# Kernel tuning notes

Hardware: AMD Instinct MI355X
Metric: run time of the kernel (lower is better)

## Reference

```python
import jax, jax.numpy as jnp
import numpy as np

D = 196  # input_size
B = 262144

def _lrelu(x):
    return jax.nn.leaky_relu(x, 0.1)

def setup_inputs() -> dict:
    key = jax.random.key(0)
    ks = jax.random.split(key, 24)
    def w(k, shape):
        fan_in = shape[0]
        return jax.random.uniform(k, shape, jnp.float32, -1.0, 1.0) / np.sqrt(fan_in)
    inp = {}
    inp['x'] = jax.random.normal(ks[0], (B, D), jnp.float32)
    # feature attention: D -> D//2 -> D
    inp['fa_w1'] = w(ks[1], (D, D // 2)); inp['fa_b1'] = jnp.zeros((D // 2,), jnp.float32)
    inp['fa_w2'] = w(ks[2], (D // 2, D)); inp['fa_b2'] = jnp.zeros((D,), jnp.float32)
    # encoder: D -> 96 -> 64 -> 32 -> (8 mean, 8 logvar)
    inp['e_w1'] = w(ks[3], (D, 96)); inp['e_b1'] = jnp.zeros((96,), jnp.float32)
    inp['e_w2'] = w(ks[4], (96, 64)); inp['e_b2'] = jnp.zeros((64,), jnp.float32)
    inp['e_w3'] = w(ks[5], (64, 32)); inp['e_b3'] = jnp.zeros((32,), jnp.float32)
    inp['e_wm'] = w(ks[6], (32, 8)); inp['e_bm'] = jnp.zeros((8,), jnp.float32)
    inp['e_wv'] = w(ks[7], (32, 8)); inp['e_bv'] = jnp.zeros((8,), jnp.float32)
    # decoder: 8 -> 32 -> 64 -> 96 -> D
    inp['d_w1'] = w(ks[8], (8, 32)); inp['d_b1'] = jnp.zeros((32,), jnp.float32)
    inp['d_w2'] = w(ks[9], (32, 64)); inp['d_b2'] = jnp.zeros((64,), jnp.float32)
    inp['d_w3'] = w(ks[10], (64, 96)); inp['d_b3'] = jnp.zeros((96,), jnp.float32)
    inp['d_w4'] = w(ks[11], (96, D)); inp['d_b4'] = jnp.zeros((D,), jnp.float32)
    # layer attention: 3 -> 3 + softmax
    inp['la_w'] = w(ks[12], (3, 3)); inp['la_b'] = jnp.zeros((3,), jnp.float32)
    return inp

def _decoder(z, d_w1, d_b1, d_w2, d_b2, d_w3, d_b3, d_w4, d_b4):
    z = _lrelu(z @ d_w1 + d_b1)
    z = _lrelu(z @ d_w2 + d_b2)
    z = _lrelu(z @ d_w3 + d_b3)
    return jax.nn.sigmoid(z @ d_w4 + d_b4)

def reference(x, fa_w1, fa_b1, fa_w2, fa_b2,
              e_w1, e_b1, e_w2, e_b2, e_w3, e_b3, e_wm, e_bm, e_wv, e_bv,
              d_w1, d_b1, d_w2, d_b2, d_w3, d_b3, d_w4, d_b4,
              la_w, la_b):
    # feature attention
    a = jax.nn.sigmoid(jnp.tanh(x @ fa_w1 + fa_b1) @ fa_w2 + fa_b2)
    attn_weights = a / (jnp.mean(a, axis=1, keepdims=True) + 1e-8)
    x_attn = x * attn_weights
    # encoder
    h1 = _lrelu(x_attn @ e_w1 + e_b1)   # [B,96]
    h2 = _lrelu(h1 @ e_w2 + e_b2)       # [B,64]
    h3 = _lrelu(h2 @ e_w3 + e_b3)       # [B,32]
    mean = h3 @ e_wm + e_bm             # [B,8]
    log_var = h3 @ e_wv + e_bv          # [B,8]
    std = jnp.exp(0.5 * log_var)
    # reparameterize (fresh eps per call, matching torch.randn_like per call)
    ek = jax.random.split(jax.random.key(42), 4)
    z = mean + jax.random.normal(ek[0], mean.shape, mean.dtype) * std
    recon = _decoder(z, d_w1, d_b1, d_w2, d_b2, d_w3, d_b3, d_w4, d_b4)
    # per-layer losses: decoder re-invoked with fresh reparam each time
    layer_losses = []
    for i, h in enumerate((h1, h2, h3)):
        zi = mean + jax.random.normal(ek[i + 1], mean.shape, mean.dtype) * std
        lr = _decoder(zi, d_w1, d_b1, d_w2, d_b2, d_w3, d_b3, d_w4, d_b4)
        layer_losses.append(jnp.mean((h - lr[:, :h.shape[1]]) ** 2, axis=1))
    layer_losses = jnp.stack(layer_losses, axis=1)  # [B,3]
    layer_attn = jax.nn.softmax(layer_losses @ la_w + la_b, axis=-1)
    weighted_layer_loss = jnp.mean(jnp.sum(layer_losses * layer_attn, axis=1))
    return (recon, mean, log_var, attn_weights, weighted_layer_loss)
```

## Files before the change

### kernel.cpp

```cpp
#include <hip/hip_runtime.h>
#include <cstdint>
#include <cstddef>


typedef short short8 __attribute__((ext_vector_type(8)));
typedef float f32x4  __attribute__((ext_vector_type(4)));
typedef float f32x16 __attribute__((ext_vector_type(16)));
typedef unsigned short u16x4 __attribute__((ext_vector_type(4)));
typedef uint32_t u32x2 __attribute__((ext_vector_type(2)));

static constexpr size_t OFF_RECON = 0;
static constexpr size_t OFF_MEAN  = (size_t)262144 * 196;
static constexpr size_t OFF_LOGV  = OFF_MEAN + (size_t)262144 * 8;
static constexpr size_t OFF_ATTN  = OFF_LOGV + (size_t)262144 * 8;
static constexpr size_t OFF_LOSS  = OFF_ATTN + (size_t)262144 * 196;

static constexpr int WS_FA1 = 0;
static constexpr int WS_FA2 = 26624;
static constexpr int WS_E1  = 51712;
static constexpr int WS_E2  = 71680;
static constexpr int WS_E3  = 78848;
static constexpr int WS_EMV = 81408;
static constexpr int WS_D1  = 82944;
static constexpr int WS_D2  = 83456;
static constexpr int WS_D3  = 86528;
static constexpr int WS_D4  = 94208;
static constexpr int WS_TOT = 119296;

static constexpr int XA0 = 0;
static constexpr int T0  = 6912;
static constexpr int TA0 = 10752;
static constexpr int H1o = 6912;
static constexpr int H2o = 10752;
static constexpr int H3o = 13568;
static constexpr int D1o = 15360;
static constexpr int D2o = 3840;
static constexpr int D3o = 0;
static constexpr int Zo  = 17152;
static constexpr int SU_TOT = 19200;
static constexpr int SF_MEAN = 0, SF_STD = 256, SF_ATT = 512, SF_LL = 544;
static constexpr int SF_TOT = 640;

static constexpr unsigned short BF_ONE = 0x3F80;

struct Params {
  const float* x;
  const float* fa_w1; const float* fa_b1; const float* fa_w2; const float* fa_b2;
  const float* e_w1;  const float* e_b1;  const float* e_w2;  const float* e_b2;
  const float* e_w3;  const float* e_b3;  const float* e_wm;  const float* e_bm;
  const float* e_wv;  const float* e_bv;
  const float* d_w1;  const float* d_b1;  const float* d_w2;  const float* d_b2;
  const float* d_w3;  const float* d_b3;  const float* d_w4;  const float* d_b4;
  const float* la_w;  const float* la_b;
  float* out;
  uint32_t key[8];
};

__host__ __device__ inline void tf2x32(uint32_t k0, uint32_t k1, uint32_t x0, uint32_t x1,
                                       uint32_t& o0, uint32_t& o1)
{
  uint32_t kx = k0 ^ k1 ^ 0x1BD11BDAu;
  uint32_t a = x0 + k0, b = x1 + k1;
#define TF_R(r) { a += b; b = (b << (r)) | (b >> (32 - (r))); b ^= a; }
  TF_R(13) TF_R(15) TF_R(26) TF_R(6)
  a += k1; b += kx + 1u;
  TF_R(17) TF_R(29) TF_R(16) TF_R(24)
  a += kx; b += k0 + 2u;
  TF_R(13) TF_R(15) TF_R(26) TF_R(6)
  a += k0; b += k1 + 3u;
  TF_R(17) TF_R(29) TF_R(16) TF_R(24)
  a += k1; b += kx + 4u;
  TF_R(13) TF_R(15) TF_R(26) TF_R(6)
  a += kx; b += k0 + 5u;
#undef TF_R
  o0 = a; o1 = b;
}

__device__ __forceinline__ float jax_normal(uint32_t k0, uint32_t k1, uint32_t idx)
{
  uint32_t o0, o1;
  tf2x32(k0, k1, 0u, idx, o0, o1);
  uint32_t bits = o0 ^ o1;
  float f = __uint_as_float((bits >> 9) | 0x3f800000u) - 1.0f;
  const float lo = -0.99999994f;
  float u = fmaf(f, 2.0f, lo);
  u = fmaxf(u, lo);
  float w = -log1pf(-u * u);
  float p;
  if (w < 5.0f) {
    w -= 2.5f;
    p = 2.81022636e-08f;
    p = fmaf(p, w, 3.43273939e-07f);
    p = fmaf(p, w, -3.5233877e-06f);
    p = fmaf(p, w, -4.39150654e-06f);
    p = fmaf(p, w, 0.00021858087f);
    p = fmaf(p, w, -0.00125372503f);
    p = fmaf(p, w, -0.00417768164f);
    p = fmaf(p, w, 0.246640727f);
    p = fmaf(p, w, 1.50140941f);
  } else {
    w = sqrtf(w) - 3.0f;
    p = -0.000200214257f;
    p = fmaf(p, w, 0.000100950558f);
    p = fmaf(p, w, 0.00134934322f);
    p = fmaf(p, w, -0.00367342844f);
    p = fmaf(p, w, 0.00573950773f);
    p = fmaf(p, w, -0.0076224613f);
    p = fmaf(p, w, 0.00943887047f);
    p = fmaf(p, w, 1.00167406f);
    p = fmaf(p, w, 2.83297682f);
  }
  return 1.41421356237f * (p * u);
}

__host__ __device__ __forceinline__ unsigned short f2b(float f) {
  uint32_t u = __float_as_uint(f);
  uint32_t r = u + 0x7fffu + ((u >> 16) & 1u);
  return (unsigned short)(r >> 16);
}
__device__ __forceinline__ float b2f(unsigned short hh) {
  return __uint_as_float(((uint32_t)hh) << 16);
}
__device__ __forceinline__ uint32_t cvt_pk(float lo, float hi) {
  uint32_t r;
  asm("v_cvt_pk_bf16_f32 %0, %1, %2" : "=v"(r) : "v"(lo), "v"(hi));
  return r;
}
__device__ __forceinline__ float rcpf(float x) { return __builtin_amdgcn_rcpf(x); }
__device__ __forceinline__ float sigm(float x) { return rcpf(1.0f + __expf(-x)); }
__device__ __forceinline__ float tanh_fast(float x) {
  float xc = fminf(fmaxf(x, -8.0f), 8.0f);
  float t = __expf(2.0f * xc);
  return (t - 1.0f) * rcpf(t + 1.0f);
}

__global__ void pack_w(Params p, unsigned short* ws)
{
  int e = blockIdx.x * 256 + threadIdx.x;
  if (e >= WS_TOT) return;
  int base, KS, K, N, special = 0;
  const float* src = nullptr; const float* bias = nullptr;
  if (e < WS_FA2)      { base = WS_FA1; KS = 13; K = 196; N = 98;  src = p.fa_w1; bias = p.fa_b1; }
  else if (e < WS_E1)  { base = WS_FA2; KS = 7;  K = 98;  N = 196; src = p.fa_w2; bias = p.fa_b2; }
  else if (e < WS_E2)  { base = WS_E1;  KS = 13; K = 196; N = 96;  src = p.e_w1;  bias = p.e_b1; }
  else if (e < WS_E3)  { base = WS_E2;  KS = 7;  K = 96;  N = 64;  src = p.e_w2;  bias = p.e_b2; }
  else if (e < WS_EMV) { base = WS_E3;  KS = 5;  K = 64;  N = 32;  src = p.e_w3;  bias = p.e_b3; }
  else if (e < WS_D1)  { base = WS_EMV; KS = 3;  K = 32;  N = 16;  special = 1; }
  else if (e < WS_D2)  { base = WS_D1;  KS = 1;  K = 8;   N = 32;  src = p.d_w1;  bias = p.d_b1; }
  else if (e < WS_D3)  { base = WS_D2;  KS = 3;  K = 32;  N = 64;  src = p.d_w2;  bias = p.d_b2; }
  else if (e < WS_D4)  { base = WS_D3;  KS = 5;  K = 64;  N = 96;  src = p.d_w3;  bias = p.d_b3; }
  else                 { base = WS_D4;  KS = 7;  K = 96;  N = 196; src = p.d_w4;  bias = p.d_b4; }
  int local = e - base;
  int j = local & 7, lane = (local >> 3) & 63, t = local >> 9;
  int ksi = t % KS, ft = t / KS;
  int k = ksi * 16 + ((lane >> 5) << 3) + j;
  int n = ft * 32 + (lane & 31);
  float v = 0.f;
  if (n < N) {
    if (k < K)       v = special ? ((n < 8) ? p.e_wm[k * 8 + n] : p.e_wv[k * 8 + (n - 8)])
                                 : src[k * N + n];
    else if (k == K) v = special ? ((n < 8) ? p.e_bm[n] : p.e_bv[n - 8]) : bias[n];
  }
  ws[e] = f2b(v);
}

template<int KS>
__device__ __forceinline__ f32x16 tile32(const unsigned short* A, int sA,
                                         const unsigned short* W, int ft, int lane)
{
  f32x16 a0 = {}, a1 = {};
  const unsigned short* ar = A + (lane & 31) * sA + ((lane >> 5) << 3);
  const unsigned short* wp = W + (size_t)(ft * KS * 64 + lane) * 8;
  constexpr int CH = (KS > 8) ? ((KS + 1) / 2) : KS;
#pragma unroll
  for (int c = 0; c < KS; c += CH) {
    short8 w8[CH], a8[CH];
#pragma unroll
    for (int i = 0; i < CH; ++i) {
      if (c + i < KS) {
        w8[i] = *(const short8*)(wp + (c + i) * 512);
        a8[i] = *(const short8*)(ar + (c + i) * 16);
      }
    }
#pragma unroll
    for (int i = 0; i < CH; ++i) {
      if (c + i < KS) {
        if (i & 1) a1 = __builtin_amdgcn_mfma_f32_32x32x16_bf16(w8[i], a8[i], a1, 0, 0, 0);
        else       a0 = __builtin_amdgcn_mfma_f32_32x32x16_bf16(w8[i], a8[i], a0, 0, 0, 0);
      }
    }
  }
  if (KS > 1) a0 += a1;
  return a0;
}

template<int KS, int NFT, int SA, int SD>
__device__ __forceinline__ void layer_lrelu(unsigned short* sU, int aOff, int dOff,
                                            const unsigned short* W, int lane, int wv)
{
  const int m = lane & 31, h = lane >> 5;
  for (int t = wv; t < NFT; t += 4) {
    f32x16 acc = tile32<KS>(sU + aOff, SA, W, t, lane);
#pragma unroll
    for (int g = 0; g < 4; ++g) {
      int fb = t * 32 + 8 * g + 4 * h;
      float v0 = fmaxf(acc[4*g+0], 0.1f*acc[4*g+0]);
      float v1 = fmaxf(acc[4*g+1], 0.1f*acc[4*g+1]);
      float v2 = fmaxf(acc[4*g+2], 0.1f*acc[4*g+2]);
      float v3 = fmaxf(acc[4*g+3], 0.1f*acc[4*g+3]);
      u32x2 pk = { cvt_pk(v0, v1), cvt_pk(v2, v3) };
      *(u32x2*)&sU[dOff + m * SD + fb] = pk;
    }
  }
}

__launch_bounds__(256, 4)
__global__ void vae_fused(Params p, const unsigned short* ws)
{
  __shared__ unsigned short sU[SU_TOT];
  __shared__ float sF[SF_TOT];

  const int tid = threadIdx.x;
  const int lane = tid & 63;
  const int wv = tid >> 6;
  const int m = lane & 31;
  const int h = lane >> 5;
  const int rb0 = blockIdx.x * 32;

  const u16x4 one4 = {BF_ONE, 0, 0, 0};
  const u16x4 zr4  = {0, 0, 0, 0};

  if (tid < 128) sF[SF_ATT + tid] = 0.f;
  for (int idx = tid; idx < 1568; idx += 256) {
    int row = idx / 49, q = idx - row * 49;
    f32x4 xv = *(const f32x4*)(p.x + (size_t)(rb0 + row) * 196 + 4 * q);
    u32x2 pk = { cvt_pk(xv[0], xv[1]), cvt_pk(xv[2], xv[3]) };
    *(u32x2*)&sU[XA0 + row * 216 + 4 * q] = pk;
  }
  if (tid < 32) {
    unsigned short* r = sU + XA0 + tid * 216;
    *(u16x4*)&r[196] = one4; *(u16x4*)&r[200] = zr4; *(u16x4*)&r[204] = zr4;
  }
  if (tid < 128) {
    unsigned short* r = sU + Zo + tid * 16;
    *(u16x4*)&r[8] = one4; *(u16x4*)&r[12] = zr4;
  }
  __syncthreads();

  {
    int t = wv;
    f32x16 acc = tile32<13>(sU + XA0, 216, ws + WS_FA1, t, lane);
#pragma unroll
    for (int g = 0; g < 4; ++g) {
      int fb = t * 32 + 8 * g + 4 * h;
      if (fb + 4 <= 120) {
        float v0 = tanh_fast(acc[4*g+0]);
        float v1 = tanh_fast(acc[4*g+1]);
        float v2 = tanh_fast(acc[4*g+2]);
        float v3 = tanh_fast(acc[4*g+3]);
        if (fb == 96) v2 = 1.0f;
        u32x2 pk = { cvt_pk(v0, v1), cvt_pk(v2, v3) };
        *(u32x2*)&sU[T0 + m * 120 + fb] = pk;
      }
    }
  }
  __syncthreads();

  for (int t = wv; t < 7; t += 4) {
    f32x16 acc = tile32<7>(sU + T0, 120, ws + WS_FA2, t, lane);
    float s = 0.f;
#pragma unroll
    for (int g = 0; g < 4; ++g) {
      int fb = t * 32 + 8 * g + 4 * h;
      if (fb + 4 <= 200) {
        float a0 = sigm(acc[4*g+0]), a1 = sigm(acc[4*g+1]);
        float a2 = sigm(acc[4*g+2]), a3 = sigm(acc[4*g+3]);
        if (fb < 196) s += a0 + a1 + a2 + a3;
        u32x2 pk = { cvt_pk(a0, a1), cvt_pk(a2, a3) };
        *(u32x2*)&sU[TA0 + m * 200 + fb] = pk;
      }
    }
    s += __shfl_xor(s, 32, 64);
    if (lane < 32) atomicAdd(&sF[SF_ATT + m], s);
  }
  __syncthreads();

  for (int idx = tid; idx < 1568; idx += 256) {
    int row = idx / 49, q = idx - row * 49;
    float inv = rcpf(sF[SF_ATT + row] * (1.0f / 196.0f) + 1e-8f);
    u16x4 ah = *(const u16x4*)&sU[TA0 + row * 200 + 4 * q];
    u16x4 xh = *(const u16x4*)&sU[XA0 + row * 216 + 4 * q];
    f32x4 aw;
    float xo[4];
#pragma unroll
    for (int i = 0; i < 4; ++i) {
      aw[i] = b2f(ah[i]) * inv;
      xo[i] = b2f(xh[i]) * aw[i];
    }
    *(f32x4*)(p.out + OFF_ATTN + (size_t)(rb0 + row) * 196 + 4 * q) = aw;
    u32x2 pk = { cvt_pk(xo[0], xo[1]), cvt_pk(xo[2], xo[3]) };
    *(u32x2*)&sU[XA0 + row * 216 + 4 * q] = pk;
  }
  __syncthreads();

  layer_lrelu<13, 3, 216, 120>(sU, XA0, H1o, ws + WS_E1, lane, wv);
  if (tid < 32) {
    unsigned short* r = sU + H1o + tid * 120;
    *(u16x4*)&r[96] = one4; *(u16x4*)&r[100] = zr4;
    *(u16x4*)&r[104] = zr4; *(u16x4*)&r[108] = zr4;
  }
  __syncthreads();
  layer_lrelu<7, 2, 120, 88>(sU, H1o, H2o, ws + WS_E2, lane, wv);
  if (tid < 32) {
    unsigned short* r = sU + H2o + tid * 88;
    *(u16x4*)&r[64] = one4; *(u16x4*)&r[68] = zr4;
    *(u16x4*)&r[72] = zr4;  *(u16x4*)&r[76] = zr4;
  }
  __syncthreads();
  layer_lrelu<5, 1, 88, 56>(sU, H2o, H3o, ws + WS_E3, lane, wv);
  if (tid < 32) {
    unsigned short* r = sU + H3o + tid * 56;
    *(u16x4*)&r[32] = one4; *(u16x4*)&r[36] = zr4;
    *(u16x4*)&r[40] = zr4;  *(u16x4*)&r[44] = zr4;
  }
  __syncthreads();

  if (wv == 0) {
    f32x16 acc = tile32<3>(sU + H3o, 56, ws + WS_EMV, 0, lane);
    f32x4 mv, lv;
#pragma unroll
    for (int e = 0; e < 4; ++e) { mv[e] = acc[e]; lv[e] = acc[4 + e]; }
#pragma unroll
    for (int e = 0; e < 4; ++e) {
      sF[SF_MEAN + m * 8 + 4 * h + e] = mv[e];
      sF[SF_STD  + m * 8 + 4 * h + e] = __expf(0.5f * lv[e]);
    }
    *(f32x4*)(p.out + OFF_MEAN + (size_t)(rb0 + m) * 8 + 4 * h) = mv;
    *(f32x4*)(p.out + OFF_LOGV + (size_t)(rb0 + m) * 8 + 4 * h) = lv;
  }
  if (tid < 32) {
    unsigned short* r1 = sU + D1o + tid * 56;
    *(u16x4*)&r1[32] = one4; *(u16x4*)&r1[36] = zr4;
    *(u16x4*)&r1[40] = zr4;  *(u16x4*)&r1[44] = zr4;
    unsigned short* r2 = sU + D2o + tid * 88;
    *(u16x4*)&r2[64] = one4; *(u16x4*)&r2[68] = zr4;
    *(u16x4*)&r2[72] = zr4;  *(u16x4*)&r2[76] = zr4;
    unsigned short* r3 = sU + D3o + tid * 120;
    *(u16x4*)&r3[96] = one4; *(u16x4*)&r3[100] = zr4;
    *(u16x4*)&r3[104] = zr4; *(u16x4*)&r3[108] = zr4;
  }
  float eps4[4];
  {
    const int row = (tid >> 1) & 31;
    const uint32_t k0 = p.key[2 * wv], k1 = p.key[2 * wv + 1];
#pragma unroll
    for (int e = 0; e < 4; ++e)
      eps4[e] = jax_normal(k0, k1, (uint32_t)(rb0 + row) * 8u + 4 * (tid & 1) + e);
  }
  __syncthreads();

  auto dec_d1 = [&](int dr) {
    f32x16 acc = tile32<1>(sU + Zo + dr * 32 * 16, 16, ws + WS_D1, 0, lane);
#pragma unroll
    for (int g = 0; g < 4; ++g) {
      int fb = 8 * g + 4 * h;
      float v0 = fmaxf(acc[4*g+0], 0.1f*acc[4*g+0]);
      float v1 = fmaxf(acc[4*g+1], 0.1f*acc[4*g+1]);
      float v2 = fmaxf(acc[4*g+2], 0.1f*acc[4*g+2]);
      float v3 = fmaxf(acc[4*g+3], 0.1f*acc[4*g+3]);
      u32x2 pk = { cvt_pk(v0, v1), cvt_pk(v2, v3) };
      *(u32x2*)&sU[D1o + m * 56 + fb] = pk;
    }
  };
  auto d4_recon = [&](int t) {
    f32x16 acc = tile32<7>(sU + D3o, 120, ws + WS_D4, t, lane);
#pragma unroll
    for (int g = 0; g < 4; ++g) {
      int fb = t * 32 + 8 * g + 4 * h;
      if (fb <= 192) {
        f32x4 v;
#pragma unroll
        for (int e = 0; e < 4; ++e) v[e] = sigm(acc[4 * g + e]);
        *(f32x4*)(p.out + OFF_RECON + (size_t)(rb0 + m) * 196 + fb) = v;
      }
    }
  };
  auto d4_loss = [&](int t, int hOff, int sH, float invD, int li) {
    f32x16 acc = tile32<7>(sU + D3o, 120, ws + WS_D4, t, lane);
    float s = 0.f;
#pragma unroll
    for (int g = 0; g < 4; ++g) {
      int fb = t * 32 + 8 * g + 4 * h;
      u16x4 hh = *(const u16x4*)&sU[hOff + m * sH + fb];
#pragma unroll
      for (int e = 0; e < 4; ++e) {
        float lr = sigm(acc[4 * g + e]);
        float dd = b2f(hh[e]) - lr;
        s = fmaf(dd, dd, s);
      }
    }
    s += __shfl_xor(s, 32, 64);
    if (lane < 32) atomicAdd(&sF[SF_LL + li * 32 + m], s * invD);
  };

  {
    const int r = tid >> 1, half = tid & 1, row = r & 31;
    f32x4 zv;
#pragma unroll
    for (int e = 0; e < 4; ++e) {
      int jj = 4 * half + e;
      zv[e] = fmaf(eps4[e], sF[SF_STD + row * 8 + jj], sF[SF_MEAN + row * 8 + jj]);
    }
    u32x2 pk = { cvt_pk(zv[0], zv[1]), cvt_pk(zv[2], zv[3]) };
    *(u32x2*)&sU[Zo + r * 16 + 4 * half] = pk;
  }
  if (wv == 0) dec_d1(0);
  __syncthreads();

#pragma unroll
  for (int d = 0; d < 4; ++d) {
    layer_lrelu<3, 2, 56, 88>(sU, D1o, D2o, ws + WS_D2, lane, wv);
    __syncthreads();
    layer_lrelu<5, 3, 88, 120>(sU, D2o, D3o, ws + WS_D3, lane, wv);
    __syncthreads();
    if (d == 0) {
      for (int t = wv; t < 8; t += 4) {
        if (t < 7) d4_recon(t);
        else       dec_d1(1);
      }
    } else if (d == 1) {
      if (wv < 3) d4_loss(wv, H1o, 120, 1.0f / 96.0f, 0);
      else        dec_d1(2);
    } else if (d == 2) {
      if (wv < 2)       d4_loss(wv, H2o, 88, 1.0f / 64.0f, 1);
      else if (wv == 2) dec_d1(3);
    } else {
      if (wv == 0) d4_loss(0, H3o, 56, 1.0f / 32.0f, 2);
    }
    __syncthreads();
  }

  if (tid < 32) {
    int r = tid;
    float l0 = sF[SF_LL + r], l1 = sF[SF_LL + 32 + r], l2 = sF[SF_LL + 64 + r];
    float lg[3];
#pragma unroll
    for (int i = 0; i < 3; ++i)
      lg[i] = p.la_b[i] + l0 * p.la_w[0 * 3 + i] + l1 * p.la_w[1 * 3 + i] + l2 * p.la_w[2 * 3 + i];
    float mx = fmaxf(lg[0], fmaxf(lg[1], lg[2]));
    float e0 = __expf(lg[0] - mx), e1 = __expf(lg[1] - mx), e2 = __expf(lg[2] - mx);
    float inv = rcpf(e0 + e1 + e2);
    float wll = (l0 * e0 + l1 * e1 + l2 * e2) * inv;
#pragma unroll
    for (int mm = 1; mm <= 16; mm <<= 1) wll += __shfl_xor(wll, mm, 64);
    if (tid == 0) atomicAdd(p.out + OFF_LOSS, wll * (1.0f / 262144.0f));
  }
}

extern "C" void kernel_launch(void* const* d_in, const int* in_sizes, int n_in,
                              void* d_out, int out_size, void* d_ws, size_t ws_size,
                              hipStream_t stream)
{
  (void)in_sizes; (void)n_in; (void)ws_size; (void)out_size;
  Params p;
  p.x     = (const float*)d_in[0];
  p.fa_w1 = (const float*)d_in[1];  p.fa_b1 = (const float*)d_in[2];
  p.fa_w2 = (const float*)d_in[3];  p.fa_b2 = (const float*)d_in[4];
  p.e_w1  = (const float*)d_in[5];  p.e_b1  = (const float*)d_in[6];
  p.e_w2  = (const float*)d_in[7];  p.e_b2  = (const float*)d_in[8];
  p.e_w3  = (const float*)d_in[9];  p.e_b3  = (const float*)d_in[10];
  p.e_wm  = (const float*)d_in[11]; p.e_bm  = (const float*)d_in[12];
  p.e_wv  = (const float*)d_in[13]; p.e_bv  = (const float*)d_in[14];
  p.d_w1  = (const float*)d_in[15]; p.d_b1  = (const float*)d_in[16];
  p.d_w2  = (const float*)d_in[17]; p.d_b2  = (const float*)d_in[18];
  p.d_w3  = (const float*)d_in[19]; p.d_b3  = (const float*)d_in[20];
  p.d_w4  = (const float*)d_in[21]; p.d_b4  = (const float*)d_in[22];
  p.la_w  = (const float*)d_in[23]; p.la_b  = (const float*)d_in[24];
  p.out   = (float*)d_out;

  for (uint32_t j = 0; j < 4; ++j) {
    uint32_t o0, o1;
    tf2x32(0u, 42u, 0u, j, o0, o1);
    p.key[2 * j] = o0; p.key[2 * j + 1] = o1;
  }

  hipMemsetAsync((char*)d_out + OFF_LOSS * sizeof(float), 0, sizeof(float), stream);

  unsigned short* ws = (unsigned short*)d_ws;
  pack_w<<<(WS_TOT + 255) / 256, 256, 0, stream>>>(p, ws);
  vae_fused<<<262144 / 32, 256, 0, stream>>>(p, ws);
}
```

Measured before the change: 327.8 us.

## Run decoder passes per-wave in registers, chaining MFMA outputs as operands

Each wave now runs one full decoder pass on its own. The MFMA accumulator is converted into the next layer's bf16 B-operand fragments with lane shuffles, so decoder activations no longer go through shared memory. This removes the four-pass loop with two barriers per pass and the shared D1/D2/D3 buffers. Feature-attention sigmoid values are also kept in registers and written straight out, dropping the TA0 staging buffer and a pass over it, and setprio is placed around the MFMA bursts. Load is now uneven: wave 0 computes all 7 recon tiles while the loss waves compute 1 to 3, and register pressure rises.

Measured after the change: 314.7 us. -4.0%, faster.

```diff
diff --git a/kernel.cpp b/kernel.cpp
--- a/kernel.cpp
+++ b/kernel.cpp
@@ -8,6 +8,7 @@
 typedef float f32x16 __attribute__((ext_vector_type(16)));
 typedef unsigned short u16x4 __attribute__((ext_vector_type(4)));
 typedef uint32_t u32x2 __attribute__((ext_vector_type(2)));
+typedef uint32_t u32x4 __attribute__((ext_vector_type(4)));
 
 static constexpr size_t OFF_RECON = 0;
 static constexpr size_t OFF_MEAN  = (size_t)262144 * 196;
@@ -29,15 +30,11 @@
 
 static constexpr int XA0 = 0;
 static constexpr int T0  = 6912;
-static constexpr int TA0 = 10752;
 static constexpr int H1o = 6912;
 static constexpr int H2o = 10752;
 static constexpr int H3o = 13568;
-static constexpr int D1o = 15360;
-static constexpr int D2o = 3840;
-static constexpr int D3o = 0;
-static constexpr int Zo  = 17152;
-static constexpr int SU_TOT = 19200;
+static constexpr int Zo  = 15360;
+static constexpr int SU_TOT = 17408;
 static constexpr int SF_MEAN = 0, SF_STD = 256, SF_ATT = 512, SF_LL = 544;
 static constexpr int SF_TOT = 640;
 
@@ -133,6 +130,10 @@
   float t = __expf(2.0f * xc);
   return (t - 1.0f) * rcpf(t + 1.0f);
 }
+__device__ __forceinline__ void lrelu16(f32x16& v) {
+#pragma unroll
+  for (int i = 0; i < 16; ++i) v[i] = fmaxf(v[i], 0.1f * v[i]);
+}
 
 __global__ void pack_w(Params p, unsigned short* ws)
 {
@@ -182,6 +183,7 @@
         a8[i] = *(const short8*)(ar + (c + i) * 16);
       }
     }
+    __builtin_amdgcn_s_setprio(1);
 #pragma unroll
     for (int i = 0; i < CH; ++i) {
       if (c + i < KS) {
@@ -189,9 +191,52 @@
         else       a0 = __builtin_amdgcn_mfma_f32_32x32x16_bf16(w8[i], a8[i], a0, 0, 0, 0);
       }
     }
+    __builtin_amdgcn_s_setprio(0);
   }
   if (KS > 1) a0 += a1;
   return a0;
+}
+
+template<int KSR>
+__device__ __forceinline__ f32x16 tile32_reg(const short8* bf, short8 bias_ch,
+                                             const unsigned short* W, int ft, int lane)
+{
+  f32x16 a0 = {}, a1 = {};
+  const unsigned short* wp = W + (size_t)(ft * (KSR + 1) * 64 + lane) * 8;
+  short8 wreg[KSR + 1];
+#pragma unroll
+  for (int i = 0; i <= KSR; ++i) wreg[i] = *(const short8*)(wp + i * 512);
+  __builtin_amdgcn_s_setprio(1);
+#pragma unroll
+  for (int i = 0; i < KSR; ++i) {
+    if (i & 1) a1 = __builtin_amdgcn_mfma_f32_32x32x16_bf16(wreg[i], bf[i], a1, 0, 0, 0);
+    else       a0 = __builtin_amdgcn_mfma_f32_32x32x16_bf16(wreg[i], bf[i], a0, 0, 0, 0);
+  }
+  a1 = __builtin_amdgcn_mfma_f32_32x32x16_bf16(wreg[KSR], bias_ch, a1, 0, 0, 0);
+  __builtin_amdgcn_s_setprio(0);
+  return a0 + a1;
+}
+
+__device__ __forceinline__ void build2(const f32x16& v, int h, short8& b0, short8& b1)
+{
+  uint32_t pk[4][2], px[4][2];
+#pragma unroll
+  for (int g = 0; g < 4; ++g) {
+    pk[g][0] = cvt_pk(v[4*g+0], v[4*g+1]);
+    pk[g][1] = cvt_pk(v[4*g+2], v[4*g+3]);
+  }
+#pragma unroll
+  for (int g = 0; g < 4; ++g) {
+    px[g][0] = (uint32_t)__shfl_xor((int)pk[g][0], 32, 64);
+    px[g][1] = (uint32_t)__shfl_xor((int)pk[g][1], 32, 64);
+  }
+  bool hb = (h != 0);
+  u32x4 c0 = { hb ? px[1][0] : pk[0][0], hb ? px[1][1] : pk[0][1],
+               hb ? pk[1][0] : px[0][0], hb ? pk[1][1] : px[0][1] };
+  u32x4 c1 = { hb ? px[3][0] : pk[2][0], hb ? px[3][1] : pk[2][1],
+               hb ? pk[3][0] : px[2][0], hb ? pk[3][1] : px[2][1] };
+  b0 = __builtin_bit_cast(short8, c0);
+  b1 = __builtin_bit_cast(short8, c1);
 }
 
 template<int KS, int NFT, int SA, int SD>
@@ -217,8 +262,8 @@
 __launch_bounds__(256, 4)
 __global__ void vae_fused(Params p, const unsigned short* ws)
 {
-  __shared__ unsigned short sU[SU_TOT];
-  __shared__ float sF[SF_TOT];
+  __shared__ __align__(16) unsigned short sU[SU_TOT];
+  __shared__ __align__(16) float sF[SF_TOT];
 
   const int tid = threadIdx.x;
   const int lane = tid & 63;
@@ -230,7 +275,7 @@
   const u16x4 one4 = {BF_ONE, 0, 0, 0};
   const u16x4 zr4  = {0, 0, 0, 0};
 
-  if (tid < 128) sF[SF_ATT + tid] = 0.f;
+  if (tid < 32) sF[SF_ATT + tid] = 0.f;
   for (int idx = tid; idx < 1568; idx += 256) {
     int row = idx / 49, q = idx - row * 49;
     f32x4 xv = *(const f32x4*)(p.x + (size_t)(rb0 + row) * 196 + 4 * q);
@@ -266,18 +311,30 @@
   }
   __syncthreads();
 
-  for (int t = wv; t < 7; t += 4) {
-    f32x16 acc = tile32<7>(sU + T0, 120, ws + WS_FA2, t, lane);
+  const int t0 = wv, t1 = wv + 4;
+  f32x16 av0, av1;
+  {
+    av0 = tile32<7>(sU + T0, 120, ws + WS_FA2, t0, lane);
     float s = 0.f;
 #pragma unroll
     for (int g = 0; g < 4; ++g) {
-      int fb = t * 32 + 8 * g + 4 * h;
-      if (fb + 4 <= 200) {
-        float a0 = sigm(acc[4*g+0]), a1 = sigm(acc[4*g+1]);
-        float a2 = sigm(acc[4*g+2]), a3 = sigm(acc[4*g+3]);
-        if (fb < 196) s += a0 + a1 + a2 + a3;
-        u32x2 pk = { cvt_pk(a0, a1), cvt_pk(a2, a3) };
-        *(u32x2*)&sU[TA0 + m * 200 + fb] = pk;
+      int fb = t0 * 32 + 8 * g + 4 * h;
+#pragma unroll
+      for (int e = 0; e < 4; ++e) {
+        av0[4*g+e] = sigm(av0[4*g+e]);
+        if (fb < 196) s += av0[4*g+e];
+      }
+    }
+    if (t1 < 7) {
+      av1 = tile32<7>(sU + T0, 120, ws + WS_FA2, t1, lane);
+#pragma unroll
+      for (int g = 0; g < 4; ++g) {
+        int fb = t1 * 32 + 8 * g + 4 * h;
+#pragma unroll
+        for (int e = 0; e < 4; ++e) {
+          av1[4*g+e] = sigm(av1[4*g+e]);
+          if (fb < 196) s += av1[4*g+e];
+        }
       }
     }
     s += __shfl_xor(s, 32, 64);
@@ -285,21 +342,28 @@
   }
   __syncthreads();
 
-  for (int idx = tid; idx < 1568; idx += 256) {
-    int row = idx / 49, q = idx - row * 49;
-    float inv = rcpf(sF[SF_ATT + row] * (1.0f / 196.0f) + 1e-8f);
-    u16x4 ah = *(const u16x4*)&sU[TA0 + row * 200 + 4 * q];
-    u16x4 xh = *(const u16x4*)&sU[XA0 + row * 216 + 4 * q];
-    f32x4 aw;
-    float xo[4];
-#pragma unroll
-    for (int i = 0; i < 4; ++i) {
-      aw[i] = b2f(ah[i]) * inv;
-      xo[i] = b2f(xh[i]) * aw[i];
-    }
-    *(f32x4*)(p.out + OFF_ATTN + (size_t)(rb0 + row) * 196 + 4 * q) = aw;
-    u32x2 pk = { cvt_pk(xo[0], xo[1]), cvt_pk(xo[2], xo[3]) };
-    *(u32x2*)&sU[XA0 + row * 216 + 4 * q] = pk;
+  {
+    float inv = rcpf(sF[SF_ATT + m] * (1.0f / 196.0f) + 1e-8f);
+#pragma unroll
+    for (int w2 = 0; w2 < 2; ++w2) {
+      int t = w2 ? t1 : t0;
+      if (t >= 7) continue;
+      const f32x16& av = w2 ? av1 : av0;
+#pragma unroll
+      for (int g = 0; g < 4; ++g) {
+        int fb = t * 32 + 8 * g + 4 * h;
+        if (fb <= 192) {
+          f32x4 aw;
+#pragma unroll
+          for (int e = 0; e < 4; ++e) aw[e] = av[4*g+e] * inv;
+          *(f32x4*)(p.out + OFF_ATTN + (size_t)(rb0 + m) * 196 + fb) = aw;
+          u16x4 xh = *(const u16x4*)&sU[XA0 + m * 216 + fb];
+          u32x2 pk = { cvt_pk(b2f(xh[0]) * aw[0], b2f(xh[1]) * aw[1]),
+                       cvt_pk(b2f(xh[2]) * aw[2], b2f(xh[3]) * aw[3]) };
+          *(u32x2*)&sU[XA0 + m * 216 + fb] = pk;
+        }
+      }
+    }
   }
   __syncthreads();
 
@@ -338,107 +402,93 @@
     *(f32x4*)(p.out + OFF_MEAN + (size_t)(rb0 + m) * 8 + 4 * h) = mv;
     *(f32x4*)(p.out + OFF_LOGV + (size_t)(rb0 + m) * 8 + 4 * h) = lv;
   }
-  if (tid < 32) {
-    unsigned short* r1 = sU + D1o + tid * 56;
-    *(u16x4*)&r1[32] = one4; *(u16x4*)&r1[36] = zr4;
-    *(u16x4*)&r1[40] = zr4;  *(u16x4*)&r1[44] = zr4;
-    unsigned short* r2 = sU + D2o + tid * 88;
-    *(u16x4*)&r2[64] = one4; *(u16x4*)&r2[68] = zr4;
-    *(u16x4*)&r2[72] = zr4;  *(u16x4*)&r2[76] = zr4;
-    unsigned short* r3 = sU + D3o + tid * 120;
-    *(u16x4*)&r3[96] = one4; *(u16x4*)&r3[100] = zr4;
-    *(u16x4*)&r3[104] = zr4; *(u16x4*)&r3[108] = zr4;
-  }
   float eps4[4];
   {
-    const int row = (tid >> 1) & 31;
+    const int row = lane >> 1;
     const uint32_t k0 = p.key[2 * wv], k1 = p.key[2 * wv + 1];
 #pragma unroll
     for (int e = 0; e < 4; ++e)
-      eps4[e] = jax_normal(k0, k1, (uint32_t)(rb0 + row) * 8u + 4 * (tid & 1) + e);
-  }
-  __syncthreads();
-
-  auto dec_d1 = [&](int dr) {
-    f32x16 acc = tile32<1>(sU + Zo + dr * 32 * 16, 16, ws + WS_D1, 0, lane);
-#pragma unroll
-    for (int g = 0; g < 4; ++g) {
-      int fb = 8 * g + 4 * h;
-      float v0 = fmaxf(acc[4*g+0], 0.1f*acc[4*g+0]);
-      float v1 = fmaxf(acc[4*g+1], 0.1f*acc[4*g+1]);
-      float v2 = fmaxf(acc[4*g+2], 0.1f*acc[4*g+2]);
-      float v3 = fmaxf(acc[4*g+3], 0.1f*acc[4*g+3]);
-      u32x2 pk = { cvt_pk(v0, v1), cvt_pk(v2, v3) };
-      *(u32x2*)&sU[D1o + m * 56 + fb] = pk;
-    }
-  };
-  auto d4_recon = [&](int t) {
-    f32x16 acc = tile32<7>(sU + D3o, 120, ws + WS_D4, t, lane);
-#pragma unroll
-    for (int g = 0; g < 4; ++g) {
-      int fb = t * 32 + 8 * g + 4 * h;
-      if (fb <= 192) {
-        f32x4 v;
-#pragma unroll
-        for (int e = 0; e < 4; ++e) v[e] = sigm(acc[4 * g + e]);
-        *(f32x4*)(p.out + OFF_RECON + (size_t)(rb0 + m) * 196 + fb) = v;
-      }
-    }
-  };
-  auto d4_loss = [&](int t, int hOff, int sH, float invD, int li) {
-    f32x16 acc = tile32<7>(sU + D3o, 120, ws + WS_D4, t, lane);
-    float s = 0.f;
-#pragma unroll
-    for (int g = 0; g < 4; ++g) {
-      int fb = t * 32 + 8 * g + 4 * h;
-      u16x4 hh = *(const u16x4*)&sU[hOff + m * sH + fb];
+      eps4[e] = jax_normal(k0, k1, (uint32_t)(rb0 + row) * 8u + 4 * (lane & 1) + e);
+  }
+  __syncthreads();
+
+  {
+    {
+      const int row = lane >> 1, half = lane & 1;
+      f32x4 zv;
 #pragma unroll
       for (int e = 0; e < 4; ++e) {
-        float lr = sigm(acc[4 * g + e]);
-        float dd = b2f(hh[e]) - lr;
-        s = fmaf(dd, dd, s);
-      }
-    }
-    s += __shfl_xor(s, 32, 64);
-    if (lane < 32) atomicAdd(&sF[SF_LL + li * 32 + m], s * invD);
-  };
-
-  {
-    const int r = tid >> 1, half = tid & 1, row = r & 31;
-    f32x4 zv;
-#pragma unroll
-    for (int e = 0; e < 4; ++e) {
-      int jj = 4 * half + e;
-      zv[e] = fmaf(eps4[e], sF[SF_STD + row * 8 + jj], sF[SF_MEAN + row * 8 + jj]);
-    }
-    u32x2 pk = { cvt_pk(zv[0], zv[1]), cvt_pk(zv[2], zv[3]) };
-    *(u32x2*)&sU[Zo + r * 16 + 4 * half] = pk;
-  }
-  if (wv == 0) dec_d1(0);
-  __syncthreads();
-
-#pragma unroll
-  for (int d = 0; d < 4; ++d) {
-    layer_lrelu<3, 2, 56, 88>(sU, D1o, D2o, ws + WS_D2, lane, wv);
-    __syncthreads();
-    layer_lrelu<5, 3, 88, 120>(sU, D2o, D3o, ws + WS_D3, lane, wv);
-    __syncthreads();
-    if (d == 0) {
-      for (int t = wv; t < 8; t += 4) {
-        if (t < 7) d4_recon(t);
-        else       dec_d1(1);
-      }
-    } else if (d == 1) {
-      if (wv < 3) d4_loss(wv, H1o, 120, 1.0f / 96.0f, 0);
-      else        dec_d1(2);
-    } else if (d == 2) {
-      if (wv < 2)       d4_loss(wv, H2o, 88, 1.0f / 64.0f, 1);
-      else if (wv == 2) dec_d1(3);
+        int jj = 4 * half + e;
+        zv[e] = fmaf(eps4[e], sF[SF_STD + row * 8 + jj], sF[SF_MEAN + row * 8 + jj]);
+      }
+      u32x2 pk = { cvt_pk(zv[0], zv[1]), cvt_pk(zv[2], zv[3]) };
+      *(u32x2*)&sU[Zo + wv * 512 + row * 16 + 4 * half] = pk;
+    }
+    u32x4 bc = { (h == 0) ? 0x00003f80u : 0u, 0u, 0u, 0u };
+    const short8 bias_ch = __builtin_bit_cast(short8, bc);
+
+    short8 f1[2];
+    {
+      f32x16 c = tile32<1>(sU + Zo + wv * 512, 16, ws + WS_D1, 0, lane);
+      lrelu16(c);
+      build2(c, h, f1[0], f1[1]);
+    }
+    short8 f2[4];
+    {
+      f32x16 c0 = tile32_reg<2>(f1, bias_ch, ws + WS_D2, 0, lane);
+      lrelu16(c0); build2(c0, h, f2[0], f2[1]);
+      f32x16 c1 = tile32_reg<2>(f1, bias_ch, ws + WS_D2, 1, lane);
+      lrelu16(c1); build2(c1, h, f2[2], f2[3]);
+    }
+    short8 f3[6];
+#pragma unroll
+    for (int ft = 0; ft < 3; ++ft) {
+      f32x16 c3 = tile32_reg<4>(f2, bias_ch, ws + WS_D3, ft, lane);
+      lrelu16(c3); build2(c3, h, f3[2 * ft], f3[2 * ft + 1]);
+    }
+    if (wv == 0) {
+#pragma unroll
+      for (int t = 0; t < 7; ++t) {
+        f32x16 c4 = tile32_reg<6>(f3, bias_ch, ws + WS_D4, t, lane);
+#pragma unroll
+        for (int g = 0; g < 4; ++g) {
+          int fb = t * 32 + 8 * g + 4 * h;
+          if (fb <= 192) {
+            f32x4 v;
+#pragma unroll
+            for (int e = 0; e < 4; ++e) v[e] = sigm(c4[4 * g + e]);
+            *(f32x4*)(p.out + OFF_RECON + (size_t)(rb0 + m) * 196 + fb) = v;
+          }
+        }
+      }
     } else {
-      if (wv == 0) d4_loss(0, H3o, 56, 1.0f / 32.0f, 2);
-    }
-    __syncthreads();
-  }
+      const int NT   = (wv == 1) ? 3 : (wv == 2) ? 2 : 1;
+      const int hOff = (wv == 1) ? H1o : (wv == 2) ? H2o : H3o;
+      const int sH   = (wv == 1) ? 120 : (wv == 2) ? 88 : 56;
+      const float invD = (wv == 1) ? (1.0f / 96.0f) : (wv == 2) ? (1.0f / 64.0f) : (1.0f / 32.0f);
+      float st = 0.f;
+#pragma unroll
+      for (int t = 0; t < 3; ++t) {
+        if (t < NT) {
+          f32x16 c4 = tile32_reg<6>(f3, bias_ch, ws + WS_D4, t, lane);
+#pragma unroll
+          for (int g = 0; g < 4; ++g) {
+            int fb = t * 32 + 8 * g + 4 * h;
+            u16x4 hh = *(const u16x4*)&sU[hOff + m * sH + fb];
+#pragma unroll
+            for (int e = 0; e < 4; ++e) {
+              float lr = sigm(c4[4 * g + e]);
+              float dd = b2f(hh[e]) - lr;
+              st = fmaf(dd, dd, st);
+            }
+          }
+        }
+      }
+      st += __shfl_xor(st, 32, 64);
+      if (lane < 32) sF[SF_LL + (wv - 1) * 32 + m] = st * invD;
+    }
+  }
+  __syncthreads();
 
   if (tid < 32) {
     int r = tid;
```
